# Kernel optimization log

Measured on AMD Instinct MI355X. Metric: run time of the kernel, lower is better.

The kernel has to match this reference:

```python
import jax, jax.numpy as jnp
import numpy as np

B, C, HEADS, W, Hh = 8, 512, 8, 32, 32
D = C // HEADS  # 64 per-head dim
N = W * Hh      # 1024 spatial tokens


def setup_inputs() -> dict:
    key = jax.random.key(0)
    ks = jax.random.split(key, 10)
    s = 1.0 / np.sqrt(C)
    return {
        "x": jax.random.normal(ks[0], (B, C, W, Hh), dtype=jnp.float32),
        "Wq": jax.random.normal(ks[1], (C, C), dtype=jnp.float32) * s,
        "bq": jax.random.normal(ks[2], (C,), dtype=jnp.float32) * 0.01,
        "Wk": jax.random.normal(ks[3], (C, C), dtype=jnp.float32) * s,
        "bk": jax.random.normal(ks[4], (C,), dtype=jnp.float32) * 0.01,
        "Wv": jax.random.normal(ks[5], (C, C), dtype=jnp.float32) * s,
        "bv": jax.random.normal(ks[6], (C,), dtype=jnp.float32) * 0.01,
        "rel_h": jax.random.normal(ks[7], (1, HEADS, D, 1, Hh), dtype=jnp.float32),
        "rel_w": jax.random.normal(ks[8], (1, HEADS, D, W, 1), dtype=jnp.float32),
    }


def reference(x, Wq, bq, Wk, bk, Wv, bv, rel_h, rel_w):
    b = x.shape[0]
    xf = x.reshape(b, C, N)  # [B, C, N] — 1x1 conv == per-position linear
    proj = lambda Wm, bm: (jnp.einsum('oc,bcn->bon', Wm, xf) + bm[None, :, None]).reshape(b, HEADS, D, N)
    q = proj(Wq, bq)  # [B, H, D, N]
    k = proj(Wk, bk)
    v = proj(Wv, bv)
    # content-content: q^T k -> [B, H, N, N]
    cc = jnp.einsum('bhdn,bhdm->bhnm', q, k)
    # relative position bias: (rel_h + rel_w) -> [H, D, N], then rel^T @ q
    rel = (rel_h + rel_w).reshape(HEADS, D, N)
    cp = jnp.einsum('hdn,bhdm->bhnm', rel, q)  # [B, H, N, N]
    attn = jax.nn.softmax(cc + cp, axis=-1)
    # out = v @ attn^T : out[d,m] = sum_n v[d,n] * attn[m,n]
    out = jnp.einsum('bhdn,bhmn->bhdm', v, attn)  # [B, H, D, N]
    return out.reshape(b, C, W, Hh)
```

## Files before the change

kernel.cpp:

```cpp
#include <hip/hip_runtime.h>

typedef _Float16 half8 __attribute__((ext_vector_type(8)));
typedef _Float16 half4 __attribute__((ext_vector_type(4)));
typedef float f32x4 __attribute__((ext_vector_type(4)));

__device__ __forceinline__ void glds16(const void* g, void* l) {
    __builtin_amdgcn_global_load_lds(
        (const __attribute__((address_space(1))) unsigned int*)g,
        (__attribute__((address_space(3))) unsigned int*)l, 16, 0, 0);
}


__global__ void k_prep_all(const float* __restrict__ Wq, const float* __restrict__ Wk,
                           const float* __restrict__ Wv, const float* __restrict__ bq,
                           const float* __restrict__ bk, const float* __restrict__ bv,
                           const float* __restrict__ x, const float* __restrict__ rel_h,
                           const float* __restrict__ rel_w, _Float16* __restrict__ Wf,
                           float* __restrict__ bias2, _Float16* __restrict__ xTf,
                           _Float16* __restrict__ rel2) {
    __shared__ float xs[64][65];
    int bid = blockIdx.x;
    if (bid < 384) {
        int t = bid * 256 + threadIdx.x;
        int m = t >> 6;
        int c8 = (t & 63) << 3;
        const float* src = (m < 512) ? (Wq + m * 512)
                         : (m < 1024 ? (Wk + (m - 512) * 512) : (Wv + (m - 1024) * 512));
        float4 v0 = *(const float4*)(src + c8);
        float4 v1 = *(const float4*)(src + c8 + 4);
        half8 o;
        o[0] = (_Float16)v0.x; o[1] = (_Float16)v0.y; o[2] = (_Float16)v0.z; o[3] = (_Float16)v0.w;
        o[4] = (_Float16)v1.x; o[5] = (_Float16)v1.y; o[6] = (_Float16)v1.z; o[7] = (_Float16)v1.w;
        *(half8*)(Wf + (size_t)m * 512 + c8) = o;
        if (t < 1536)
            bias2[t] = (t < 512) ? bq[t] : (t < 1024 ? bk[t - 512] : bv[t - 1024]);
    } else if (bid < 1408) {
        int i = bid - 384;
        int nt = (i & 15) << 6, ct = ((i >> 4) & 7) << 6, b = i >> 7;
        int t = threadIdx.x;
        const float* xb = x + ((size_t)b * 512 + ct) * 1024 + nt;
#pragma unroll
        for (int p = 0; p < 4; ++p) {
            int c = p * 16 + (t >> 4), n4 = (t & 15) * 4;
            float4 v = *(const float4*)(xb + (size_t)c * 1024 + n4);
            xs[c][n4] = v.x; xs[c][n4 + 1] = v.y; xs[c][n4 + 2] = v.z; xs[c][n4 + 3] = v.w;
        }
        __syncthreads();
        int nl = t >> 2, part = t & 3;
        _Float16* rowp = xTf + ((size_t)b * 1024 + nt + nl) * 512;
#pragma unroll
        for (int g = 0; g < 2; ++g) {
            half8 o;
#pragma unroll
            for (int j = 0; j < 8; ++j)
                o[j] = (_Float16)xs[part * 16 + g * 8 + j][nl];
            *(half8*)(rowp + ct + part * 16 + g * 8) = o;
        }
    } else {
        int tid = (bid - 1408) * 256 + threadIdx.x;
        int h = tid >> 13;
        int rem = tid & 8191;
        int n = rem >> 3;
        int g = rem & 7;
        int hh = n & 31, ww = n >> 5;
        half8 o;
#pragma unroll
        for (int j = 0; j < 8; ++j) {
            int d = g * 8 + j;
            o[j] = (_Float16)(rel_h[(h * 64 + d) * 32 + hh] + rel_w[(h * 64 + d) * 32 + ww]);
        }
        *(half8*)(rel2 + ((size_t)h * 1024 + n) * 64 + g * 8) = o;
    }
}

__global__ __launch_bounds__(256, 3) void k_proj(const _Float16* __restrict__ Wf,
                                                 const _Float16* __restrict__ xTf,
                                                 const float* __restrict__ bias2,
                                                 _Float16* __restrict__ q2,
                                                 _Float16* __restrict__ k2,
                                                 _Float16* __restrict__ vb) {
    __shared__ __align__(16) _Float16 As[8192];
    __shared__ __align__(16) _Float16 Bs[8192];
    int t = threadIdx.x;
    int lane = t & 63, w = t >> 6;
    int lm = lane & 15, lq = lane >> 4;
    int wr = (w >> 1) * 64, wc = (w & 1) * 64;
    int mb = blockIdx.y * 128, nb = blockIdx.x * 128, b = blockIdx.z;
    int rl = lane >> 2;
    int csw = ((lane & 3) ^ ((lane >> 3) & 3)) * 8;
    const _Float16* Ag0 = Wf + (size_t)(mb + w * 32 + rl) * 512 + csw;
    const _Float16* Ag1 = Ag0 + 16 * 512;
    const _Float16* Bg0 = xTf + ((size_t)b * 1024 + nb + w * 32 + rl) * 512 + csw;
    const _Float16* Bg1 = Bg0 + 16 * 512;
    f32x4 acc[4][4];
#pragma unroll
    for (int i = 0; i < 4; ++i)
#pragma unroll
        for (int j = 0; j < 4; ++j) acc[i][j] = {0.f, 0.f, 0.f, 0.f};
    int fsw = (lq ^ ((lm >> 1) & 3)) * 8;
    for (int k0 = 0; k0 < 512; k0 += 64) {
#pragma unroll
        for (int kh = 0; kh < 2; ++kh) {
            int ko = k0 + kh * 32;
            glds16(Ag0 + ko, &As[kh * 4096 + (w * 32) * 32]);
            glds16(Ag1 + ko, &As[kh * 4096 + (w * 32 + 16) * 32]);
            glds16(Bg0 + ko, &Bs[kh * 4096 + (w * 32) * 32]);
            glds16(Bg1 + ko, &Bs[kh * 4096 + (w * 32 + 16) * 32]);
        }
        __syncthreads();
#pragma unroll
        for (int kh = 0; kh < 2; ++kh) {
            half8 af[4], bfr[4];
#pragma unroll
            for (int mt = 0; mt < 4; ++mt)
                af[mt] = *(half8*)&As[kh * 4096 + (wr + mt * 16 + lm) * 32 + fsw];
#pragma unroll
            for (int nt = 0; nt < 4; ++nt)
                bfr[nt] = *(half8*)&Bs[kh * 4096 + (wc + nt * 16 + lm) * 32 + fsw];
#pragma unroll
            for (int mt = 0; mt < 4; ++mt)
#pragma unroll
                for (int nt = 0; nt < 4; ++nt)
                    acc[mt][nt] = __builtin_amdgcn_mfma_f32_16x16x32_f16(af[mt], bfr[nt], acc[mt][nt], 0, 0, 0);
        }
        __syncthreads();
    }
    int sect = mb >> 9;
    int hloc = ((mb & 511) + wr) >> 6;
    size_t bh = (size_t)b * 8 + hloc;
    if (sect < 2) {
        float sc = (sect == 0) ? 1.44269504089f : 1.0f;
        _Float16* dst = (sect == 0 ? q2 : k2) + bh * 1024 * 64;
#pragma unroll
        for (int mt = 0; mt < 4; ++mt) {
            int d0 = mt * 16 + lq * 4;
            float bi0 = bias2[mb + wr + d0];
            float bi1 = bias2[mb + wr + d0 + 1];
            float bi2 = bias2[mb + wr + d0 + 2];
            float bi3 = bias2[mb + wr + d0 + 3];
#pragma unroll
            for (int nt = 0; nt < 4; ++nt) {
                int n = nb + wc + nt * 16 + lm;
                half4 o;
                o[0] = (_Float16)((acc[mt][nt][0] + bi0) * sc);
                o[1] = (_Float16)((acc[mt][nt][1] + bi1) * sc);
                o[2] = (_Float16)((acc[mt][nt][2] + bi2) * sc);
                o[3] = (_Float16)((acc[mt][nt][3] + bi3) * sc);
                *(half4*)(dst + (size_t)n * 64 + d0) = o;
            }
        }
    } else {
        _Float16* dst = vb + bh * 64 * 1024;
#pragma unroll
        for (int mt = 0; mt < 4; ++mt)
#pragma unroll
            for (int reg = 0; reg < 4; ++reg) {
                int d = mt * 16 + lq * 4 + reg;
                float bi = bias2[mb + wr + d];
#pragma unroll
                for (int nt = 0; nt < 4; ++nt) {
                    int n = nb + wc + nt * 16 + lm;
                    dst[(size_t)d * 1024 + n] = (_Float16)(acc[mt][nt][reg] + bi);
                }
            }
    }
}

__global__ __launch_bounds__(256, 3) void k_attn(const _Float16* __restrict__ q2,
                                                 const _Float16* __restrict__ k2,
                                                 const _Float16* __restrict__ rel2,
                                                 const _Float16* __restrict__ vb,
                                                 float* __restrict__ out) {
    __shared__ __align__(16) char pool[45056];
    _Float16* kb_s = (_Float16*)pool;
    _Float16* v_s  = (_Float16*)(pool + 17408);
    _Float16* p_s  = (_Float16*)(pool + 26624);
    int t = threadIdx.x;
    int lane = t & 63, w = t >> 6;
    int lm = lane & 15, lq = lane >> 4;
    int lin = blockIdx.x;
    int mt0 = lin >> 6;
    int bh_ = lin & 63;
    int h = bh_ & 7, b = bh_ >> 3;
    size_t bh = (size_t)b * 8 + h;
    const _Float16* q2b = q2 + bh * 1024 * 64;
    const _Float16* k2b = k2 + bh * 1024 * 64;
    const _Float16* relb = rel2 + (size_t)h * 1024 * 64;
    const _Float16* vbb = vb + bh * 64 * 1024;
    float* outb = out + bh * 64 * 1024 + mt0 * 128;

    int r = t >> 2, part = t & 3;
    const _Float16* ksrc = ((part < 2) ? (k2b + part * 32) : (q2b + (part - 2) * 32));
    int vc = (t & 3) * 16;
    const _Float16* vsrcb = vbb + (size_t)r * 1024 + vc;
    _Float16* kdst = kb_s + r * 136 + part * 32;
    _Float16* vdst = v_s + r * 72 + vc;

    uint4 kc0, kc1, kc2, kc3, vv0, vv1;
    {
        const uint4* s_ = (const uint4*)(ksrc + (size_t)r * 64);
        kc0 = s_[0]; kc1 = s_[1]; kc2 = s_[2]; kc3 = s_[3];
        const uint4* v_ = (const uint4*)vsrcb;
        vv0 = v_[0]; vv1 = v_[1];
    }

    {
        int n = mt0 * 128 + r;
        const _Float16* src = (part < 2) ? (q2b + (size_t)n * 64 + part * 32)
                                         : (relb + (size_t)n * 64 + (part - 2) * 32);
        ((uint4*)kdst)[0] = ((const uint4*)src)[0];
        ((uint4*)kdst)[1] = ((const uint4*)src)[1];
        ((uint4*)kdst)[2] = ((const uint4*)src)[2];
        ((uint4*)kdst)[3] = ((const uint4*)src)[3];
    }
    __syncthreads();
    half8 ah0[4], ah1[4];
#pragma unroll
    for (int kk = 0; kk < 4; ++kk)
        ah0[kk] = *(half8*)&kb_s[(w * 16 + lm) * 136 + kk * 32 + lq * 8];
    __syncthreads();
    {
        int n = mt0 * 128 + 64 + r;
        const _Float16* src = (part < 2) ? (q2b + (size_t)n * 64 + part * 32)
                                         : (relb + (size_t)n * 64 + (part - 2) * 32);
        ((uint4*)kdst)[0] = ((const uint4*)src)[0];
        ((uint4*)kdst)[1] = ((const uint4*)src)[1];
        ((uint4*)kdst)[2] = ((const uint4*)src)[2];
        ((uint4*)kdst)[3] = ((const uint4*)src)[3];
    }
    __syncthreads();
#pragma unroll
    for (int kk = 0; kk < 4; ++kk)
        ah1[kk] = *(half8*)&kb_s[(w * 16 + lm) * 136 + kk * 32 + lq * 8];
    __syncthreads();

    f32x4 acco0[4], acco1[4];
#pragma unroll
    for (int i = 0; i < 4; ++i) { acco0[i] = {0.f, 0.f, 0.f, 0.f}; acco1[i] = {0.f, 0.f, 0.f, 0.f}; }
    float mrun0 = -3e38f, lrun0 = 0.f, mrun1 = -3e38f, lrun1 = 0.f;

    for (int kt = 0; kt < 16; ++kt) {
        ((uint4*)kdst)[0] = kc0;
        ((uint4*)kdst)[1] = kc1;
        ((uint4*)kdst)[2] = kc2;
        ((uint4*)kdst)[3] = kc3;
        ((uint4*)vdst)[0] = vv0;
        ((uint4*)vdst)[1] = vv1;
        __syncthreads();
        int nn = ((kt + 1) & 15) * 64;
        const uint4* s_ = (const uint4*)(ksrc + (size_t)(nn + r) * 64);
        uint4 kn0 = s_[0], kn1 = s_[1], kn2 = s_[2], kn3 = s_[3];
        const uint4* v_ = (const uint4*)(vsrcb + nn);
        uint4 vn0 = v_[0], vn1 = v_[1];
        f32x4 s0[4], s1[4];
#pragma unroll
        for (int ct = 0; ct < 4; ++ct) { s0[ct] = {0.f, 0.f, 0.f, 0.f}; s1[ct] = {0.f, 0.f, 0.f, 0.f}; }
#pragma unroll
        for (int ct = 0; ct < 4; ++ct) {
            half8 kf[4];
#pragma unroll
            for (int kk = 0; kk < 4; ++kk)
                kf[kk] = *(half8*)&kb_s[(ct * 16 + lm) * 136 + kk * 32 + lq * 8];
#pragma unroll
            for (int kk = 0; kk < 4; ++kk) {
                s0[ct] = __builtin_amdgcn_mfma_f32_16x16x32_f16(kf[kk], ah0[kk], s0[ct], 0, 0, 0);
                s1[ct] = __builtin_amdgcn_mfma_f32_16x16x32_f16(kf[kk], ah1[kk], s1[ct], 0, 0, 0);
            }
        }
        {
            float mx = -3e38f;
#pragma unroll
            for (int ct = 0; ct < 4; ++ct)
#pragma unroll
                for (int reg = 0; reg < 4; ++reg) mx = fmaxf(mx, s0[ct][reg]);
            mx = fmaxf(mx, __shfl_xor(mx, 16));
            mx = fmaxf(mx, __shfl_xor(mx, 32));
            float mnew = fmaxf(mrun0, mx);
            float al_ = exp2f(mrun0 - mnew);
            float rs = 0.f;
#pragma unroll
            for (int ct = 0; ct < 4; ++ct) {
                float p0 = exp2f(s0[ct][0] - mnew);
                float p1 = exp2f(s0[ct][1] - mnew);
                float p2 = exp2f(s0[ct][2] - mnew);
                float p3 = exp2f(s0[ct][3] - mnew);
                rs += (p0 + p1) + (p2 + p3);
                half4 o; o[0] = (_Float16)p0; o[1] = (_Float16)p1; o[2] = (_Float16)p2; o[3] = (_Float16)p3;
                *(half4*)&p_s[(w * 16 + lm) * 72 + ct * 16 + lq * 4] = o;
            }
            rs += __shfl_xor(rs, 16);
            rs += __shfl_xor(rs, 32);
            lrun0 = lrun0 * al_ + rs;
            mrun0 = mnew;
#pragma unroll
            for (int dt = 0; dt < 4; ++dt) {
                acco0[dt][0] *= al_; acco0[dt][1] *= al_;
                acco0[dt][2] *= al_; acco0[dt][3] *= al_;
            }
        }
        {
            float mx = -3e38f;
#pragma unroll
            for (int ct = 0; ct < 4; ++ct)
#pragma unroll
                for (int reg = 0; reg < 4; ++reg) mx = fmaxf(mx, s1[ct][reg]);
            mx = fmaxf(mx, __shfl_xor(mx, 16));
            mx = fmaxf(mx, __shfl_xor(mx, 32));
            float mnew = fmaxf(mrun1, mx);
            float al_ = exp2f(mrun1 - mnew);
            float rs = 0.f;
#pragma unroll
            for (int ct = 0; ct < 4; ++ct) {
                float p0 = exp2f(s1[ct][0] - mnew);
                float p1 = exp2f(s1[ct][1] - mnew);
                float p2 = exp2f(s1[ct][2] - mnew);
                float p3 = exp2f(s1[ct][3] - mnew);
                rs += (p0 + p1) + (p2 + p3);
                half4 o; o[0] = (_Float16)p0; o[1] = (_Float16)p1; o[2] = (_Float16)p2; o[3] = (_Float16)p3;
                *(half4*)&p_s[(64 + w * 16 + lm) * 72 + ct * 16 + lq * 4] = o;
            }
            rs += __shfl_xor(rs, 16);
            rs += __shfl_xor(rs, 32);
            lrun1 = lrun1 * al_ + rs;
            mrun1 = mnew;
#pragma unroll
            for (int dt = 0; dt < 4; ++dt) {
                acco1[dt][0] *= al_; acco1[dt][1] *= al_;
                acco1[dt][2] *= al_; acco1[dt][3] *= al_;
            }
        }
        half8 p0f[2], p1f[2];
#pragma unroll
        for (int ch = 0; ch < 2; ++ch) {
            p0f[ch] = *(half8*)&p_s[(w * 16 + lm) * 72 + ch * 32 + lq * 8];
            p1f[ch] = *(half8*)&p_s[(64 + w * 16 + lm) * 72 + ch * 32 + lq * 8];
        }
#pragma unroll
        for (int dt = 0; dt < 4; ++dt) {
            half8 vf0 = *(half8*)&v_s[(dt * 16 + lm) * 72 + lq * 8];
            half8 vf1 = *(half8*)&v_s[(dt * 16 + lm) * 72 + 32 + lq * 8];
            acco0[dt] = __builtin_amdgcn_mfma_f32_16x16x32_f16(vf0, p0f[0], acco0[dt], 0, 0, 0);
            acco0[dt] = __builtin_amdgcn_mfma_f32_16x16x32_f16(vf1, p0f[1], acco0[dt], 0, 0, 0);
            acco1[dt] = __builtin_amdgcn_mfma_f32_16x16x32_f16(vf0, p1f[0], acco1[dt], 0, 0, 0);
            acco1[dt] = __builtin_amdgcn_mfma_f32_16x16x32_f16(vf1, p1f[1], acco1[dt], 0, 0, 0);
        }
        __syncthreads();
        kc0 = kn0; kc1 = kn1; kc2 = kn2; kc3 = kn3;
        vv0 = vn0; vv1 = vn1;
    }
    float li0 = 1.f / lrun0, li1 = 1.f / lrun1;
#pragma unroll
    for (int dt = 0; dt < 4; ++dt)
#pragma unroll
        for (int reg = 0; reg < 4; ++reg) {
            int d = dt * 16 + lq * 4 + reg;
            outb[(size_t)d * 1024 + w * 16 + lm] = acco0[dt][reg] * li0;
            outb[(size_t)d * 1024 + 64 + w * 16 + lm] = acco1[dt][reg] * li1;
        }
}

extern "C" void kernel_launch(void* const* d_in, const int* in_sizes, int n_in,
                              void* d_out, int out_size, void* d_ws, size_t ws_size,
                              hipStream_t stream) {
    const float* x     = (const float*)d_in[0];
    const float* Wq    = (const float*)d_in[1];
    const float* bq    = (const float*)d_in[2];
    const float* Wk    = (const float*)d_in[3];
    const float* bk    = (const float*)d_in[4];
    const float* Wv    = (const float*)d_in[5];
    const float* bv    = (const float*)d_in[6];
    const float* rel_h = (const float*)d_in[7];
    const float* rel_w = (const float*)d_in[8];
    char* ws = (char*)d_ws;
    _Float16* Wf   = (_Float16*)(ws);
    float* bias2   = (float*)(ws + 1572864);
    _Float16* xTf  = (_Float16*)(ws + 1579008);
    _Float16* q2   = (_Float16*)(ws + 9967616);
    _Float16* k2   = (_Float16*)(ws + 18356224);
    _Float16* vb   = (_Float16*)(ws + 26744832);
    _Float16* rel2 = (_Float16*)(ws + 35133440);
    float* out = (float*)d_out;

    hipLaunchKernelGGL(k_prep_all, dim3(1664),     dim3(256), 0, stream,
                       Wq, Wk, Wv, bq, bk, bv, x, rel_h, rel_w, Wf, bias2, xTf, rel2);
    hipLaunchKernelGGL(k_proj,     dim3(8, 12, 8), dim3(256), 0, stream, Wf, xTf, bias2, q2, k2, vb);
    hipLaunchKernelGGL(k_attn,     dim3(512),      dim3(256), 0, stream, q2, k2, rel2, vb, out);
}
```

Before: 153.0 us.

## Stage projection epilogue through LDS and double-buffer K/V tiles in attention

```diff
diff --git a/kernel.cpp b/kernel.cpp
--- a/kernel.cpp
+++ b/kernel.cpp
@@ -79,8 +79,10 @@
                                                  _Float16* __restrict__ q2,
                                                  _Float16* __restrict__ k2,
                                                  _Float16* __restrict__ vb) {
-    __shared__ __align__(16) _Float16 As[8192];
-    __shared__ __align__(16) _Float16 Bs[8192];
+    __shared__ __align__(16) char pool[34816];
+    _Float16* As = (_Float16*)pool;
+    _Float16* Bs = (_Float16*)(pool + 16384);
+    _Float16* ts = (_Float16*)pool;
     int t = threadIdx.x;
     int lane = t & 63, w = t >> 6;
     int lm = lane & 15, lq = lane >> 4;
@@ -126,55 +128,71 @@
         __syncthreads();
     }
     int sect = mb >> 9;
-    int hloc = ((mb & 511) + wr) >> 6;
-    size_t bh = (size_t)b * 8 + hloc;
+    int h0 = (mb & 511) >> 6;
+    float sc = (sect == 0) ? 1.44269504089f : 1.0f;
+#pragma unroll
+    for (int mt = 0; mt < 4; ++mt) {
+        int d0 = wr + mt * 16 + lq * 4;
+        float bi0 = bias2[mb + d0];
+        float bi1 = bias2[mb + d0 + 1];
+        float bi2 = bias2[mb + d0 + 2];
+        float bi3 = bias2[mb + d0 + 3];
+#pragma unroll
+        for (int nt = 0; nt < 4; ++nt) {
+            int n = wc + nt * 16 + lm;
+            half4 o;
+            o[0] = (_Float16)((acc[mt][nt][0] + bi0) * sc);
+            o[1] = (_Float16)((acc[mt][nt][1] + bi1) * sc);
+            o[2] = (_Float16)((acc[mt][nt][2] + bi2) * sc);
+            o[3] = (_Float16)((acc[mt][nt][3] + bi3) * sc);
+            *(half4*)&ts[n * 136 + d0] = o;
+        }
+    }
+    __syncthreads();
     if (sect < 2) {
-        float sc = (sect == 0) ? 1.44269504089f : 1.0f;
-        _Float16* dst = (sect == 0 ? q2 : k2) + bh * 1024 * 64;
-#pragma unroll
-        for (int mt = 0; mt < 4; ++mt) {
-            int d0 = mt * 16 + lq * 4;
-            float bi0 = bias2[mb + wr + d0];
-            float bi1 = bias2[mb + wr + d0 + 1];
-            float bi2 = bias2[mb + wr + d0 + 2];
-            float bi3 = bias2[mb + wr + d0 + 3];
-#pragma unroll
-            for (int nt = 0; nt < 4; ++nt) {
-                int n = nb + wc + nt * 16 + lm;
-                half4 o;
-                o[0] = (_Float16)((acc[mt][nt][0] + bi0) * sc);
-                o[1] = (_Float16)((acc[mt][nt][1] + bi1) * sc);
-                o[2] = (_Float16)((acc[mt][nt][2] + bi2) * sc);
-                o[3] = (_Float16)((acc[mt][nt][3] + bi3) * sc);
-                *(half4*)(dst + (size_t)n * 64 + d0) = o;
+        _Float16* base = (sect == 0 ? q2 : k2);
+#pragma unroll
+        for (int hh = 0; hh < 2; ++hh) {
+            size_t bh = (size_t)b * 8 + h0 + hh;
+            _Float16* dst = base + (bh * 1024 + nb) * 64;
+#pragma unroll
+            for (int i = 0; i < 4; ++i) {
+                int u = i * 256 + t;
+                int n = u >> 3, c = u & 7;
+                *(uint4*)(dst + (size_t)n * 64 + c * 8) = *(uint4*)&ts[n * 136 + hh * 64 + c * 8];
             }
         }
     } else {
-        _Float16* dst = vb + bh * 64 * 1024;
-#pragma unroll
-        for (int mt = 0; mt < 4; ++mt)
-#pragma unroll
-            for (int reg = 0; reg < 4; ++reg) {
-                int d = mt * 16 + lq * 4 + reg;
-                float bi = bias2[mb + wr + d];
-#pragma unroll
-                for (int nt = 0; nt < 4; ++nt) {
-                    int n = nb + wc + nt * 16 + lm;
-                    dst[(size_t)d * 1024 + n] = (_Float16)(acc[mt][nt][reg] + bi);
-                }
-            }
+#pragma unroll
+        for (int hh = 0; hh < 2; ++hh) {
+            size_t bh = (size_t)b * 8 + h0 + hh;
+            _Float16* dst = vb + bh * 64 * 1024 + nb;
+#pragma unroll
+            for (int i = 0; i < 4; ++i) {
+                int u = i * 256 + t;
+                int d = u >> 4, c = u & 15;
+                half8 o;
+#pragma unroll
+                for (int j = 0; j < 8; ++j)
+                    o[j] = ts[(c * 8 + j) * 136 + hh * 64 + d];
+                *(half8*)(dst + (size_t)d * 1024 + c * 8) = o;
+            }
+        }
     }
 }
 
-__global__ __launch_bounds__(256, 3) void k_attn(const _Float16* __restrict__ q2,
+__global__ __launch_bounds__(256, 2) void k_attn(const _Float16* __restrict__ q2,
                                                  const _Float16* __restrict__ k2,
                                                  const _Float16* __restrict__ rel2,
                                                  const _Float16* __restrict__ vb,
                                                  float* __restrict__ out) {
-    __shared__ __align__(16) char pool[45056];
-    _Float16* kb_s = (_Float16*)pool;
-    _Float16* v_s  = (_Float16*)(pool + 17408);
-    _Float16* p_s  = (_Float16*)(pool + 26624);
+    __shared__ __align__(16) char pool[71680];
+    _Float16* kb0 = (_Float16*)pool;
+    _Float16* kb1 = (_Float16*)(pool + 17408);
+    _Float16* v0s = (_Float16*)(pool + 34816);
+    _Float16* v1s = (_Float16*)(pool + 44032);
+    _Float16* p_s = (_Float16*)(pool + 53248);
+    _Float16* aa  = (_Float16*)pool;
     int t = threadIdx.x;
     int lane = t & 63, w = t >> 6;
     int lm = lane & 15, lq = lane >> 4;
@@ -193,8 +211,8 @@
     const _Float16* ksrc = ((part < 2) ? (k2b + part * 32) : (q2b + (part - 2) * 32));
     int vc = (t & 3) * 16;
     const _Float16* vsrcb = vbb + (size_t)r * 1024 + vc;
-    _Float16* kdst = kb_s + r * 136 + part * 32;
-    _Float16* vdst = v_s + r * 72 + vc;
+    int koff = r * 136 + part * 32;
+    int voff = r * 72 + vc;
 
     uint4 kc0, kc1, kc2, kc3, vv0, vv1;
     {
@@ -204,35 +222,37 @@
         vv0 = v_[0]; vv1 = v_[1];
     }
 
-    {
-        int n = mt0 * 128 + r;
+#pragma unroll
+    for (int rr = 0; rr < 2; ++rr) {
+        int row = rr * 64 + r;
+        int n = mt0 * 128 + row;
         const _Float16* src = (part < 2) ? (q2b + (size_t)n * 64 + part * 32)
                                          : (relb + (size_t)n * 64 + (part - 2) * 32);
-        ((uint4*)kdst)[0] = ((const uint4*)src)[0];
-        ((uint4*)kdst)[1] = ((const uint4*)src)[1];
-        ((uint4*)kdst)[2] = ((const uint4*)src)[2];
-        ((uint4*)kdst)[3] = ((const uint4*)src)[3];
+        _Float16* dst = aa + row * 136 + part * 32;
+        ((uint4*)dst)[0] = ((const uint4*)src)[0];
+        ((uint4*)dst)[1] = ((const uint4*)src)[1];
+        ((uint4*)dst)[2] = ((const uint4*)src)[2];
+        ((uint4*)dst)[3] = ((const uint4*)src)[3];
     }
     __syncthreads();
     half8 ah0[4], ah1[4];
 #pragma unroll
-    for (int kk = 0; kk < 4; ++kk)
-        ah0[kk] = *(half8*)&kb_s[(w * 16 + lm) * 136 + kk * 32 + lq * 8];
+    for (int kk = 0; kk < 4; ++kk) {
+        ah0[kk] = *(half8*)&aa[(w * 16 + lm) * 136 + kk * 32 + lq * 8];
+        ah1[kk] = *(half8*)&aa[(64 + w * 16 + lm) * 136 + kk * 32 + lq * 8];
+    }
     __syncthreads();
     {
-        int n = mt0 * 128 + 64 + r;
-        const _Float16* src = (part < 2) ? (q2b + (size_t)n * 64 + part * 32)
-                                         : (relb + (size_t)n * 64 + (part - 2) * 32);
-        ((uint4*)kdst)[0] = ((const uint4*)src)[0];
-        ((uint4*)kdst)[1] = ((const uint4*)src)[1];
-        ((uint4*)kdst)[2] = ((const uint4*)src)[2];
-        ((uint4*)kdst)[3] = ((const uint4*)src)[3];
-    }
-    __syncthreads();
-#pragma unroll
-    for (int kk = 0; kk < 4; ++kk)
-        ah1[kk] = *(half8*)&kb_s[(w * 16 + lm) * 136 + kk * 32 + lq * 8];
-    __syncthreads();
+        _Float16* kd = kb0 + koff;
+        ((uint4*)kd)[0] = kc0; ((uint4*)kd)[1] = kc1;
+        ((uint4*)kd)[2] = kc2; ((uint4*)kd)[3] = kc3;
+        _Float16* vd = v0s + voff;
+        ((uint4*)vd)[0] = vv0; ((uint4*)vd)[1] = vv1;
+        const uint4* s_ = (const uint4*)(ksrc + (size_t)(64 + r) * 64);
+        kc0 = s_[0]; kc1 = s_[1]; kc2 = s_[2]; kc3 = s_[3];
+        const uint4* v_ = (const uint4*)(vsrcb + 64);
+        vv0 = v_[0]; vv1 = v_[1];
+    }
 
     f32x4 acco0[4], acco1[4];
 #pragma unroll
@@ -240,14 +260,19 @@
     float mrun0 = -3e38f, lrun0 = 0.f, mrun1 = -3e38f, lrun1 = 0.f;
 
     for (int kt = 0; kt < 16; ++kt) {
-        ((uint4*)kdst)[0] = kc0;
-        ((uint4*)kdst)[1] = kc1;
-        ((uint4*)kdst)[2] = kc2;
-        ((uint4*)kdst)[3] = kc3;
-        ((uint4*)vdst)[0] = vv0;
-        ((uint4*)vdst)[1] = vv1;
         __syncthreads();
-        int nn = ((kt + 1) & 15) * 64;
+        _Float16* kcur = (kt & 1) ? kb1 : kb0;
+        _Float16* vcur = (kt & 1) ? v1s : v0s;
+        _Float16* kw   = (kt & 1) ? kb0 : kb1;
+        _Float16* vw   = (kt & 1) ? v0s : v1s;
+        {
+            _Float16* kd = kw + koff;
+            ((uint4*)kd)[0] = kc0; ((uint4*)kd)[1] = kc1;
+            ((uint4*)kd)[2] = kc2; ((uint4*)kd)[3] = kc3;
+            _Float16* vd = vw + voff;
+            ((uint4*)vd)[0] = vv0; ((uint4*)vd)[1] = vv1;
+        }
+        int nn = ((kt + 2) & 15) * 64;
         const uint4* s_ = (const uint4*)(ksrc + (size_t)(nn + r) * 64);
         uint4 kn0 = s_[0], kn1 = s_[1], kn2 = s_[2], kn3 = s_[3];
         const uint4* v_ = (const uint4*)(vsrcb + nn);
@@ -260,7 +285,7 @@
             half8 kf[4];
 #pragma unroll
             for (int kk = 0; kk < 4; ++kk)
-                kf[kk] = *(half8*)&kb_s[(ct * 16 + lm) * 136 + kk * 32 + lq * 8];
+                kf[kk] = *(half8*)&kcur[(ct * 16 + lm) * 136 + kk * 32 + lq * 8];
 #pragma unroll
             for (int kk = 0; kk < 4; ++kk) {
                 s0[ct] = __builtin_amdgcn_mfma_f32_16x16x32_f16(kf[kk], ah0[kk], s0[ct], 0, 0, 0);
@@ -337,14 +362,13 @@
         }
 #pragma unroll
         for (int dt = 0; dt < 4; ++dt) {
-            half8 vf0 = *(half8*)&v_s[(dt * 16 + lm) * 72 + lq * 8];
-            half8 vf1 = *(half8*)&v_s[(dt * 16 + lm) * 72 + 32 + lq * 8];
+            half8 vf0 = *(half8*)&vcur[(dt * 16 + lm) * 72 + lq * 8];
+            half8 vf1 = *(half8*)&vcur[(dt * 16 + lm) * 72 + 32 + lq * 8];
             acco0[dt] = __builtin_amdgcn_mfma_f32_16x16x32_f16(vf0, p0f[0], acco0[dt], 0, 0, 0);
             acco0[dt] = __builtin_amdgcn_mfma_f32_16x16x32_f16(vf1, p0f[1], acco0[dt], 0, 0, 0);
             acco1[dt] = __builtin_amdgcn_mfma_f32_16x16x32_f16(vf0, p1f[0], acco1[dt], 0, 0, 0);
             acco1[dt] = __builtin_amdgcn_mfma_f32_16x16x32_f16(vf1, p1f[1], acco1[dt], 0, 0, 0);
         }
-        __syncthreads();
         kc0 = kn0; kc1 = kn1; kc2 = kn2; kc3 = kn3;
         vv0 = vn0; vv1 = vn1;
     }
```

Measured after the change: 156.1 us. 2.0% more time.
